# Optimization experiments

Measured on AMD Instinct MI355X. Metric: run time of the kernel, lower is better.

## Reference

```python
import jax, jax.numpy as jnp
from jax import lax
import numpy as np

# pywt db5 decomposition low-pass filter
_DB5 = np.array([0.003335725285001549, -0.012580751999015526, -0.006241490213011705,
                 0.07757149384006515, -0.03224486958502952, -0.24229488706619015,
                 0.13842814590110342, 0.7243085284385744, 0.6038292697974729,
                 0.160102397974125], dtype=np.float32)
_L = 10       # filter length (db5)
_LEVELS = 5   # decomp_level
_NT = 15      # SURE tuning grid size


def _filters():
    dec_lo = jnp.asarray(_DB5)
    sign = jnp.asarray(((-1.0) ** (np.arange(_L) + 1)).astype(np.float32))
    dec_hi = sign * dec_lo[::-1]          # QMF: g[k] = (-1)^(k+1) h[L-1-k]
    return dec_lo, dec_hi, dec_lo[::-1], dec_hi[::-1]


def _dwt1d(x, dlo, dhi):
    # x: (B, N) -> (B, 2, floor((N+L-1)/2)); pywt 'symmetric' convention
    p = _L - 1
    xe = jnp.pad(x, ((0, 0), (p, p)), mode='symmetric')[:, 1:]
    k = jnp.stack([dlo[::-1], dhi[::-1]])[:, None, :]  # (2,1,L), true convolution
    return lax.conv_general_dilated(xe[:, None, :], k, (2,), 'VALID',
                                    dimension_numbers=('NCH', 'OIH', 'NCH'))


def _idwt1d(a, d, rlo, rhi, n_out):
    # a,d: (B, M) -> (B, n_out); zero-upsample via lhs_dilation, full conv, crop L-2
    k = jnp.stack([rlo[::-1], rhi[::-1]])[None, :, :]  # (1,2,L)
    y = lax.conv_general_dilated(jnp.stack([a, d], axis=1), k, (1,),
                                 [(_L - 1, _L - 1)], lhs_dilation=(2,),
                                 dimension_numbers=('NCH', 'OIH', 'NCH'))
    return y[:, 0, _L - 2:_L - 2 + n_out]


def _dwt2_level(x, dlo, dhi):
    # x: (C, H, W) -> ll (C,Hd,Wd), highs (C,3,Hd,Wd)
    C, H, W = x.shape
    yw = _dwt1d(x.reshape(C * H, W), dlo, dhi).reshape(C, H, 2, -1)
    Wd = yw.shape[-1]
    yw = yw.transpose(0, 2, 3, 1)  # (C, wband, Wd, H)
    yh = _dwt1d(yw.reshape(C * 2 * Wd, H), dlo, dhi).reshape(C, 2, Wd, 2, -1)
    yh = yh.transpose(0, 1, 3, 4, 2)  # (C, wband, hband, Hd, Wd)
    ll = yh[:, 0, 0]
    highs = jnp.stack([yh[:, 0, 1], yh[:, 1, 0], yh[:, 1, 1]], axis=1)
    return ll, highs


def _idwt2_level(ll, highs, rlo, rhi, h_out, w_out):
    C, Hd, Wd = ll.shape
    lh, hl, hh = highs[:, 0], highs[:, 1], highs[:, 2]

    def inv_h(a, d):  # inverse along H axis
        at = a.transpose(0, 2, 1).reshape(C * Wd, Hd)
        dt = d.transpose(0, 2, 1).reshape(C * Wd, Hd)
        r = _idwt1d(at, dt, rlo, rhi, h_out)
        return r.reshape(C, Wd, h_out).transpose(0, 2, 1)

    lo_w = inv_h(ll, lh)
    hi_w = inv_h(hl, hh)
    r = _idwt1d(lo_w.reshape(C * h_out, Wd), hi_w.reshape(C * h_out, Wd),
                rlo, rhi, w_out)
    return r.reshape(C, h_out, w_out)


def _est_additive_noise(data):
    eps = 1e-6
    C = data.shape[0]
    ddp = data @ data.T
    ddpi = jnp.linalg.inv(ddp + eps * jnp.eye(C, dtype=data.dtype))

    def per_band(i):
        xx = ddpi - jnp.outer(ddpi[:, i], ddpi[i, :]) / ddpi[i, i]
        ddpa = ddp[:, i].at[i].set(0.0)
        beta = (xx @ ddpa).at[i].set(0.0)
        return data[i] - beta @ data

    return jax.vmap(per_band)(jnp.arange(C))


def _hyres(x, min_iter):
    dlo, dhi, rlo, rhi = _filters()
    H, W, C = x.shape
    N = H * W
    # 1) noise estimation -> per-band noise power omega1
    w = _est_additive_noise(x.reshape(N, C).T)               # (C, N)
    omega1 = (jnp.sqrt(jnp.var(w, axis=1, ddof=1)) + 1e-30) ** 2  # (C,)
    y_w = x * omega1 ** -0.5
    # 2) PCA: y_w2d = (U*S) @ Vh ; pc = scores as image cube
    u, s, vh = jnp.linalg.svd(y_w.reshape(N, C), full_matrices=False)
    pc = (u * s).reshape(H, W, C).transpose(2, 0, 1)         # (C, H, W)
    # 3) multi-level 2D DWT per band
    xmax, xmin = x.max(), x.min()
    ll = pc
    highs, sizes = [], []
    for _ in range(_LEVELS):
        sizes.append(ll.shape[1:])
        ll, hi = _dwt2_level(ll, dlo, dhi)
        highs.append(hi)
    ll = jnp.nan_to_num(ll, nan=0.0, posinf=xmax, neginf=xmin)
    highs = [jnp.nan_to_num(h, nan=0.0, posinf=xmax, neginf=xmin) for h in highs]
    # 4) flatten all coefficients -> (M, C)
    flat = [ll.reshape(C, -1)] + [h.reshape(C, -1) for h in highs]
    vperm = jnp.concatenate(flat, axis=1).T
    M = vperm.shape[0]
    norm2 = jnp.sum(vperm * vperm)
    K = norm2 - float(M * C)
    # 5) per-band SURE over a fixed threshold grid (vectorized over bands)
    x2 = vperm ** 2
    t_max = float(np.sqrt(np.log(M)))
    t_grid = jnp.linspace(0.0, t_max, _NT)

    def sure_at(t):
        t2 = t * t
        cnt = jnp.sum(x2 >= t2, axis=0).astype(vperm.dtype)
        sm = jnp.sum(jnp.minimum(x2, t2), axis=0)
        return sm + 2.0 * cnt - float(M)

    sure_all = jax.vmap(sure_at)(t_grid)                     # (NT, C)
    # 6) cumulative SURE recurrence S_r = sum_{j<r} S_j + a_r + K ; min over grid

    def step(cum, a_r):
        s_r = cum + a_r + K
        return cum + s_r, jnp.min(s_r)

    _, min_sure = lax.scan(step, jnp.zeros(_NT, vperm.dtype), sure_all.T)
    prev = jnp.concatenate([min_sure[:1], min_sure[:-1]])
    idx = jnp.arange(C)
    cond = (idx > min_iter) & jnp.logical_not(min_sure > 2.0 * prev)
    rank = jnp.where(jnp.any(cond), jnp.argmax(cond), C - 1)
    # 7) keep bands < rank (zeroing == slicing since iDWT/matmul are per-band linear)
    keep = (idx < rank).astype(vperm.dtype)
    ll_k = ll * keep[:, None, None]
    highs_k = [h * keep[:, None, None, None] for h in highs]
    y_est = ll_k
    for hi, (h_out, w_out) in zip(reversed(highs_k), reversed(sizes)):
        y_est = _idwt2_level(y_est, hi, rlo, rhi, h_out, w_out)
    y2d = y_est.transpose(1, 2, 0).reshape(N, C)
    y_restored = ((omega1 ** 0.5) * (y2d @ vh).reshape(H, W, C))
    return y_restored


def setup_inputs() -> dict:
    key = jax.random.key(0)
    x = jax.random.uniform(key, (256, 256, 191), dtype=jnp.float32)
    return {"x": x, "min_iter": 2}


def reference(x, min_iter):
    return _hyres(x, min_iter)
```

## Files before the change

kernel.cpp:

```cpp
#include <hip/hip_runtime.h>
#include <math.h>
#include <cstdint>

#define CH 191
#define NPIX 65536
#define MCOEF 74287
#define CSTRIDE 74288
#define SW32 4
#define NSKEW (96 * 194)

__device__ const float g_dlo[10] = {
  0.003335725285001549f, -0.012580751999015526f, -0.006241490213011705f,
  0.07757149384006515f, -0.03224486958502952f, -0.24229488706619015f,
  0.13842814590110342f, 0.7243085284385744f, 0.6038292697974729f,
  0.160102397974125f };
__device__ const float g_dhi[10] = {
  -0.160102397974125f, 0.6038292697974729f, -0.7243085284385744f,
  0.13842814590110342f, 0.24229488706619015f, -0.03224486958502952f,
  -0.07757149384006515f, -0.006241490213011705f, 0.012580751999015526f,
  0.003335725285001549f };

struct TArgs { double t2[15]; };

__device__ __forceinline__ int sk(int a, int b) {
  int s = a + b; if (s >= CH) s -= CH;
  int d = a - b; if (d < 0) d = -d;
  int df = (d > 95) ? (CH - d) : d;
  return df * 194 + s;
}

#define BAR_LGKM() asm volatile("s_waitcnt lgkmcnt(0)\n\ts_barrier" ::: "memory")

__global__ __launch_bounds__(256) void k_ddp(const float* __restrict__ x,
                                             double* __restrict__ ddp) {
  __shared__ float as[32][33];
  __shared__ float bs[32][33];
  int i0 = blockIdx.x * 32, j0 = blockIdx.y * 32;
  if (j0 < i0) return;
  int t = threadIdx.x;
  int n0 = blockIdx.z * 4096;
  int tx = t & 15, ty = t >> 4;
  double a00 = 0, a01 = 0, a10 = 0, a11 = 0;
  for (int nb = 0; nb < 4096; nb += 32) {
    for (int e = t; e < 1024; e += 256) {
      int kk = e >> 5, ii = e & 31;
      int n = n0 + nb + kk;
      as[kk][ii] = (i0 + ii < CH) ? x[(size_t)n * CH + i0 + ii] : 0.f;
      bs[kk][ii] = (j0 + ii < CH) ? x[(size_t)n * CH + j0 + ii] : 0.f;
    }
    __syncthreads();
    #pragma unroll 8
    for (int kk = 0; kk < 32; ++kk) {
      double x0 = as[kk][tx], x1 = as[kk][tx + 16];
      double y0 = bs[kk][ty], y1 = bs[kk][ty + 16];
      a00 += x0 * y0; a01 += x0 * y1; a10 += x1 * y0; a11 += x1 * y1;
    }
    __syncthreads();
  }
  int i = i0 + tx, j = j0 + ty;
  if (i < CH) {
    if (j < CH)      atomicAdd(&ddp[i * CH + j], a00);
    if (j + 16 < CH) atomicAdd(&ddp[i * CH + j + 16], a01);
  }
  if (i + 16 < CH) {
    if (j < CH)      atomicAdd(&ddp[(i + 16) * CH + j], a10);
    if (j + 16 < CH) atomicAdd(&ddp[(i + 16) * CH + j + 16], a11);
  }
}

__global__ void k_mirror(double* __restrict__ ddp) {
  int e = blockIdx.x * 256 + threadIdx.x;
  if (e >= CH * CH) return;
  int i = e / CH, j = e % CH;
  if (i > j) ddp[e] = ddp[j * CH + i];
}

__global__ __launch_bounds__(256) void k_rsum(const float* __restrict__ x,
                                              double* __restrict__ rsum) {
  int t = threadIdx.x;
  if (t >= CH) return;
  int row0 = blockIdx.x * 256;
  double a = 0;
  for (int r = 0; r < 256; ++r) a += (double)x[(size_t)(row0 + r) * CH + t];
  atomicAdd(&rsum[t], a);
}

__global__ __launch_bounds__(768) void k_gj(const double* __restrict__ ddp,
                                            float* __restrict__ out) {
  __shared__ float fc[192];
  int t = threadIdx.x;
  int i = t % 192;
  int cg = t / 192;
  int j0 = cg * 48;
  bool act = (i < CH);
  float a[48];
  #pragma unroll
  for (int m = 0; m < 48; ++m) {
    int j = j0 + m;
    a[m] = (act && j < CH) ? (float)(ddp[i * CH + j] + ((i == j) ? 1e-6 : 0.0)) : 0.f;
  }
  if (t < 192) fc[t] = 0.f;
  __syncthreads();
  for (int k = 0; k < CH; ++k) {
    int cgk = k / 48;
    int mk = k - cgk * 48;
    if (cg == cgk && act) {
      float v = 0.f;
      #pragma unroll
      for (int m = 0; m < 48; ++m) v = (m == mk) ? a[m] : v;
      fc[i] = v;
    }
    __syncthreads();
    float dinv = 1.0f / fc[k];
    float fci = fc[i];
    bool iskrow = (i == k);
    float s = fci * dinv;
    float colv = iskrow ? (-dinv) : s;
    #pragma unroll
    for (int mq = 0; mq < 12; ++mq) {
      float4 f4 = *(const float4*)&fc[j0 + mq * 4];
      #pragma unroll
      for (int c4 = 0; c4 < 4; ++c4) {
        int m = mq * 4 + c4;
        float fj = (c4 == 0) ? f4.x : (c4 == 1) ? f4.y : (c4 == 2) ? f4.z : f4.w;
        float gen = iskrow ? (fj * dinv) : (a[m] - s * fj);
        bool iskcol = (cg == cgk) && (m == mk);
        a[m] = iskcol ? colv : gen;
      }
    }
    __syncthreads();
  }
  if (act) {
    #pragma unroll
    for (int m = 0; m < 48; ++m) {
      int j = j0 + m;
      if (j < CH) out[i * CH + j] = -a[m];
    }
  }
}

__global__ void k_newton1(const double* __restrict__ ddp, const float* __restrict__ X,
                          double* __restrict__ T) {
  int j = blockIdx.x * 16 + threadIdx.x, i = blockIdx.y * 16 + threadIdx.y;
  if (i >= CH || j >= CH) return;
  double acc = 0;
  for (int k = 0; k < CH; ++k) {
    double a = ddp[i * CH + k] + (i == k ? 1e-6 : 0.0);
    acc += a * (double)X[k * CH + j];
  }
  T[i * CH + j] = (i == j ? 2.0 : 0.0) - acc;
}
__global__ void k_newton2(const float* __restrict__ X, const double* __restrict__ T,
                          double* __restrict__ P) {
  int j = blockIdx.x * 16 + threadIdx.x, i = blockIdx.y * 16 + threadIdx.y;
  if (i >= CH || j >= CH) return;
  double acc = 0;
  for (int k = 0; k < CH; ++k) acc += (double)X[i * CH + k] * T[k * CH + j];
  P[i * CH + j] = acc;
}

__global__ __launch_bounds__(256) void k_beta(const double* __restrict__ ddp,
                                              const double* __restrict__ P,
                                              const double* __restrict__ rsum,
                                              double* __restrict__ sqrtom,
                                              double* __restrict__ invs) {
  __shared__ double bet[CH];
  __shared__ double red[256];
  int i = blockIdx.x, t = threadIdx.x;
  double pii = P[i * CH + i];
  for (int j = t; j < CH; j += 256) {
    double pjip = P[j * CH + i] / pii;
    double acc = 0;
    for (int k = 0; k < CH; ++k) {
      double ddpa = (k == i) ? 0.0 : ddp[k * CH + i];
      acc += (P[j * CH + k] - pjip * P[i * CH + k]) * ddpa;
    }
    bet[j] = (j == i) ? 0.0 : acc;
  }
  __syncthreads();
  double s1 = 0, s2 = 0;
  for (int j = t; j < CH; j += 256) {
    double gj = ((j == i) ? 1.0 : 0.0) - bet[j];
    s1 += gj * rsum[j];
    double tj = 0;
    for (int k = 0; k < CH; ++k) {
      double gk = ((k == i) ? 1.0 : 0.0) - bet[k];
      tj += ddp[j * CH + k] * gk;
    }
    s2 += gj * tj;
  }
  red[t] = s1; __syncthreads();
  for (int o = 128; o; o >>= 1) { if (t < o) red[t] += red[t + o]; __syncthreads(); }
  double sumw = red[0]; __syncthreads();
  red[t] = s2; __syncthreads();
  for (int o = 128; o; o >>= 1) { if (t < o) red[t] += red[t + o]; __syncthreads(); }
  if (t == 0) {
    double sumsq = red[0];
    double var = (sumsq - sumw * sumw / 65536.0) / 65535.0;
    if (var < 0) var = 0;
    double so = sqrt(var) + 1e-30;
    sqrtom[i] = so;
    invs[i] = 1.0 / so;
  }
}

__global__ void k_packG(const double* __restrict__ ddp, const double* __restrict__ invs,
                        float* __restrict__ Gsk, float* __restrict__ dgf,
                        double* __restrict__ G64) {
  int e = blockIdx.x * 256 + threadIdx.x;
  if (e >= CH * CH) return;
  int i = e / CH, j = e % CH;
  double v = ddp[e] * invs[i] * invs[j];
  G64[e] = v;
  if (j >= i) Gsk[sk(i, j)] = (float)v;
  if (j == i) dgf[i] = (float)v;
}

__global__ __launch_bounds__(1024) void k_jac32(const float* __restrict__ Gsk,
                                                const float* __restrict__ dg0,
                                                float2* __restrict__ rlogA) {
  extern __shared__ float As[];
  __shared__ float2 csn[96];
  __shared__ float dg[CH];
  int t = threadIdx.x;

  int jS[5], kS[5]; int ntask = 0;
  for (int id = t; id < 4560; id += 1024) {
    int j = 0, off = 0;
    while (off + (95 - j) <= id) { off += 95 - j; ++j; }
    jS[ntask] = j; kS[ntask] = j + 1 + (id - off);
    ++ntask;
  }
  int a00[5], a01[5], a10[5], a11[5], limA[5], limB[5];
  #pragma unroll
  for (int ii = 0; ii < 5; ++ii) {
    if (ii < ntask) {
      int j = jS[ii], k = kS[ii];
      int A = j + k;
      int B = k - j;
      int dfB = (A > 95) ? (CH - A) : A;
      int bA = B * 194;
      int bB = dfB * 194;
      a00[ii] = (bA + A) * 4;
      a11[ii] = (bA + CH - A) * 4;
      a01[ii] = (bB + CH - B) * 4;
      a10[ii] = (bB + B) * 4;
      limA[ii] = (bA + CH) * 4;
      limB[ii] = (bB + CH) * 4;
    } else {
      a00[ii] = a01[ii] = a10[ii] = a11[ii] = 0;
      limA[ii] = limB[ii] = 1 << 30; jS[ii] = 0; kS[ii] = 1;
    }
  }

  for (int e = t; e < NSKEW; e += 1024) As[e] = Gsk[e];
  if (t < CH) dg[t] = dg0[t];
  __syncthreads();

  const char* Asb = (const char*)As;
  for (int sweep = 0; sweep < SW32; ++sweep) {
    for (int r = 0; r < CH; ++r) {
      float m0[5], m1[5], m2[5], m3[5];
      #pragma unroll
      for (int ii = 0; ii < 5; ++ii) {
        if (ii < ntask) {
          m0[ii] = *(const float*)(Asb + a00[ii]);
          m1[ii] = *(const float*)(Asb + a01[ii]);
          if (jS[ii] != 0) {
            m2[ii] = *(const float*)(Asb + a10[ii]);
            m3[ii] = *(const float*)(Asb + a11[ii]);
          }
        }
      }
      if (t >= 1 && t < 96) {
        int p = r + t; if (p >= CH) p -= CH;
        int q = r - t; if (q < 0) q += CH;
        int ipq = sk(p, q);
        float app = dg[p], aqq = dg[q], apq = As[ipq];
        float c = 1.0f, s = 0.0f, piv = apq, dp = app, dq = aqq;
        if (fabsf(apq) > 3e-7f * (fabsf(app) + fabsf(aqq)) + 1e-30f) {
          float tau = (aqq - app) / (2.0f * apq);
          float tt = copysignf(1.0f, tau) / (fabsf(tau) + sqrtf(1.0f + tau * tau));
          c = 1.0f / sqrtf(1.0f + tt * tt); s = tt * c;
          dp = app - tt * apq; dq = aqq + tt * apq; piv = 0.0f;
        }
        dg[p] = dp; dg[q] = dq;
        As[ipq] = piv;
        csn[t] = make_float2(c, s);
        rlogA[((size_t)(sweep * CH + r)) * 95 + (t - 1)] = make_float2(c, s);
      }
      BAR_LGKM();
      #pragma unroll
      for (int ii = 0; ii < 5; ++ii) {
        if (ii < ntask) {
          float2 ck2 = csn[kS[ii]];
          if (jS[ii] == 0) {
            float vp = m0[ii], vq = m1[ii];
            *(float*)((char*)As + a00[ii]) = ck2.x * vp - ck2.y * vq;
            *(float*)((char*)As + a01[ii]) = ck2.y * vp + ck2.x * vq;
          } else {
            float2 cj2 = csn[jS[ii]];
            float n00 = ck2.x * m0[ii] - ck2.y * m1[ii];
            float n01 = ck2.y * m0[ii] + ck2.x * m1[ii];
            float n10 = ck2.x * m2[ii] - ck2.y * m3[ii];
            float n11 = ck2.y * m2[ii] + ck2.x * m3[ii];
            *(float*)((char*)As + a00[ii]) = cj2.x * n00 - cj2.y * n10;
            *(float*)((char*)As + a10[ii]) = cj2.y * n00 + cj2.x * n10;
            *(float*)((char*)As + a01[ii]) = cj2.x * n01 - cj2.y * n11;
            *(float*)((char*)As + a11[ii]) = cj2.y * n01 + cj2.x * n11;
          }
          a00[ii] += 8; if (a00[ii] >= limA[ii]) a00[ii] -= 764;
          a11[ii] += 8; if (a11[ii] >= limA[ii]) a11[ii] -= 764;
          a01[ii] += 8; if (a01[ii] >= limB[ii]) a01[ii] -= 764;
          a10[ii] += 8; if (a10[ii] >= limB[ii]) a10[ii] -= 764;
        }
      }
      BAR_LGKM();
    }
  }
}

__global__ __launch_bounds__(128) void k_replayA(const float2* __restrict__ rlogA,
                                                 double* __restrict__ Q) {
  __shared__ double vr[CH];
  int row = blockIdx.x, t = threadIdx.x;
  const int NR = SW32 * CH;
  for (int j = t; j < CH; j += 128) vr[j] = (j == row) ? 1.0 : 0.0;
  bool act = (t < 95);
  float2 nb[4];
  #pragma unroll
  for (int u = 0; u < 4; ++u)
    nb[u] = (act && u < NR) ? rlogA[(size_t)u * 95 + t] : make_float2(1.f, 0.f);
  BAR_LGKM();
  int r = 0;
  for (int g = 0; g < NR; g += 4) {
    #pragma unroll
    for (int u = 0; u < 4; ++u) {
      float2 cur = nb[u];
      int gn = g + u + 4;
      nb[u] = (act && gn < NR) ? rlogA[(size_t)gn * 95 + t] : make_float2(1.f, 0.f);
      if (act && cur.y != 0.f) {
        int k = t + 1;
        int p = r + k; if (p >= CH) p -= CH;
        int q = r - k; if (q < 0) q += CH;
        double s = (double)cur.y;
        double c = sqrt(fmax(0.0, 1.0 - s * s));
        double vp = vr[p], vq = vr[q];
        vr[p] = c * vp - s * vq;
        vr[q] = s * vp + c * vq;
      }
      if (++r == CH) r = 0;
      BAR_LGKM();
    }
  }
  for (int j = t; j < CH; j += 128) Q[(size_t)row * CH + j] = vr[j];
}

__global__ void k_gq(const double* __restrict__ G64, const double* __restrict__ Q,
                     double* __restrict__ T) {
  int j = blockIdx.x * 16 + threadIdx.x, i = blockIdx.y * 16 + threadIdx.y;
  if (i >= CH || j >= CH) return;
  double acc = 0;
  for (int k = 0; k < CH; ++k) acc += G64[i * CH + k] * Q[(size_t)k * CH + j];
  T[i * CH + j] = acc;
}
__global__ void k_qtq(const double* __restrict__ Q, const double* __restrict__ T,
                      double* __restrict__ A2sk, double* __restrict__ dg64) {
  int j = blockIdx.x * 16 + threadIdx.x, i = blockIdx.y * 16 + threadIdx.y;
  if (i >= CH || j >= CH || j < i) return;
  double acc = 0;
  for (int k = 0; k < CH; ++k) acc += Q[(size_t)k * CH + i] * T[k * CH + j];
  if (j == i) dg64[i] = acc;
  else A2sk[sk(i, j)] = acc;
}

__global__ __launch_bounds__(1024) void k_jac64(const double* __restrict__ A2sk,
                                                const double* __restrict__ dg0,
                                                double* __restrict__ eig,
                                                double2* __restrict__ rlogB) {
  extern __shared__ double As64[];
  __shared__ double2 csn[96];
  __shared__ double dg[CH];
  int t = threadIdx.x;

  int jS[5], kS[5]; int ntask = 0;
  for (int id = t; id < 4560; id += 1024) {
    int j = 0, off = 0;
    while (off + (95 - j) <= id) { off += 95 - j; ++j; }
    jS[ntask] = j; kS[ntask] = j + 1 + (id - off);
    ++ntask;
  }
  int a00[5], a01[5], a10[5], a11[5], limA[5], limB[5];
  #pragma unroll
  for (int ii = 0; ii < 5; ++ii) {
    if (ii < ntask) {
      int j = jS[ii], k = kS[ii];
      int A = j + k;
      int B = k - j;
      int dfB = (A > 95) ? (CH - A) : A;
      int bA = B * 194;
      int bB = dfB * 194;
      a00[ii] = (bA + A) * 8;
      a11[ii] = (bA + CH - A) * 8;
      a01[ii] = (bB + CH - B) * 8;
      a10[ii] = (bB + B) * 8;
      limA[ii] = (bA + CH) * 8;
      limB[ii] = (bB + CH) * 8;
    } else {
      a00[ii] = a01[ii] = a10[ii] = a11[ii] = 0;
      limA[ii] = limB[ii] = 1 << 30; jS[ii] = 0; kS[ii] = 1;
    }
  }

  for (int e = t; e < NSKEW; e += 1024) As64[e] = A2sk[e];
  if (t < CH) dg[t] = dg0[t];
  __syncthreads();

  const char* Asb = (const char*)As64;
  for (int r = 0; r < CH; ++r) {
    double m0[5], m1[5], m2[5], m3[5];
    #pragma unroll
    for (int ii = 0; ii < 5; ++ii) {
      if (ii < ntask) {
        m0[ii] = *(const double*)(Asb + a00[ii]);
        m1[ii] = *(const double*)(Asb + a01[ii]);
        if (jS[ii] != 0) {
          m2[ii] = *(const double*)(Asb + a10[ii]);
          m3[ii] = *(const double*)(Asb + a11[ii]);
        }
      }
    }
    if (t >= 1 && t < 96) {
      int p = r + t; if (p >= CH) p -= CH;
      int q = r - t; if (q < 0) q += CH;
      int ipq = sk(p, q);
      double app = dg[p], aqq = dg[q], apq = As64[ipq];
      double c = 1.0, s = 0.0, piv = apq, dp = app, dq = aqq;
      if (fabs(apq) > 4e-16 * (fabs(app) + fabs(aqq)) + 1e-300) {
        double tau = (aqq - app) / (2.0 * apq);
        double tt = copysign(1.0, tau) / (fabs(tau) + sqrt(1.0 + tau * tau));
        c = 1.0 / sqrt(1.0 + tt * tt); s = tt * c;
        dp = app - tt * apq; dq = aqq + tt * apq; piv = 0.0;
      }
      dg[p] = dp; dg[q] = dq;
      As64[ipq] = piv;
      csn[t] = make_double2(c, s);
      rlogB[(size_t)r * 95 + (t - 1)] = make_double2(c, s);
    }
    BAR_LGKM();
    #pragma unroll
    for (int ii = 0; ii < 5; ++ii) {
      if (ii < ntask) {
        double2 ck2 = csn[kS[ii]];
        if (jS[ii] == 0) {
          double vp = m0[ii], vq = m1[ii];
          *(double*)((char*)As64 + a00[ii]) = ck2.x * vp - ck2.y * vq;
          *(double*)((char*)As64 + a01[ii]) = ck2.y * vp + ck2.x * vq;
        } else {
          double2 cj2 = csn[jS[ii]];
          double n00 = ck2.x * m0[ii] - ck2.y * m1[ii];
          double n01 = ck2.y * m0[ii] + ck2.x * m1[ii];
          double n10 = ck2.x * m2[ii] - ck2.y * m3[ii];
          double n11 = ck2.y * m2[ii] + ck2.x * m3[ii];
          *(double*)((char*)As64 + a00[ii]) = cj2.x * n00 - cj2.y * n10;
          *(double*)((char*)As64 + a10[ii]) = cj2.y * n00 + cj2.x * n10;
          *(double*)((char*)As64 + a01[ii]) = cj2.x * n01 - cj2.y * n11;
          *(double*)((char*)As64 + a11[ii]) = cj2.y * n01 + cj2.x * n11;
        }
        a00[ii] += 16; if (a00[ii] >= limA[ii]) a00[ii] -= 1528;
        a11[ii] += 16; if (a11[ii] >= limA[ii]) a11[ii] -= 1528;
        a01[ii] += 16; if (a01[ii] >= limB[ii]) a01[ii] -= 1528;
        a10[ii] += 16; if (a10[ii] >= limB[ii]) a10[ii] -= 1528;
      }
    }
    BAR_LGKM();
  }
  for (int i = t; i < CH; i += 1024) eig[i] = dg[i];
}

__global__ __launch_bounds__(128) void k_replayB(const double2* __restrict__ rlogB,
                                                 const double* __restrict__ Q,
                                                 double* __restrict__ V) {
  __shared__ double vr[CH];
  int row = blockIdx.x, t = threadIdx.x;
  const int NR = CH;
  for (int j = t; j < CH; j += 128) vr[j] = Q[(size_t)row * CH + j];
  double2 nxt = (t < 95) ? rlogB[t] : make_double2(1.0, 0.0);
  BAR_LGKM();
  for (int g = 0; g < NR; ++g) {
    double2 cur = nxt;
    if (t < 95 && g + 1 < NR) nxt = rlogB[(size_t)(g + 1) * 95 + t];
    if (t < 95 && cur.y != 0.0) {
      int k = t + 1;
      int p = g + k; if (p >= CH) p -= CH;
      int q = g - k; if (q < 0) q += CH;
      double vp = vr[p], vq = vr[q];
      vr[p] = cur.x * vp - cur.y * vq;
      vr[q] = cur.y * vp + cur.x * vq;
    }
    BAR_LGKM();
  }
  for (int j = t; j < CH; j += 128) V[(size_t)row * CH + j] = vr[j];
}

__global__ __launch_bounds__(256) void k_sortprep(const double* __restrict__ eig,
                                                  const double* __restrict__ V,
                                                  const double* __restrict__ invs,
                                                  int* __restrict__ perm,
                                                  float* __restrict__ Vw) {
  __shared__ double ev[CH];
  __shared__ int pm[CH];
  int t = threadIdx.x;
  if (t < CH) ev[t] = eig[t];
  __syncthreads();
  if (t < CH) {
    double my = ev[t];
    int rk = 0;
    for (int j = 0; j < CH; ++j) {
      double o = ev[j];
      rk += (o > my || (o == my && j < t)) ? 1 : 0;
    }
    pm[rk] = t;
  }
  __syncthreads();
  if (t < CH) perm[t] = pm[t];
  for (int e = t; e < 192 * 192; e += 256) {
    int k = e / 192, i = e - k * 192;
    float v = 0.f;
    if (k < CH && i < CH) v = (float)(invs[k] * V[(size_t)k * CH + pm[i]]);
    Vw[e] = v;
  }
}

__global__ __launch_bounds__(256) void k_pc(const float* __restrict__ x,
                                            const float* __restrict__ Vw,
                                            float* __restrict__ pcT) {
  __shared__ float xs[16][65];
  __shared__ float vs[16][33];
  int n0 = blockIdx.x * 64, i0 = blockIdx.y * 32;
  int t = threadIdx.x;
  int tn = t & 15, ti = t >> 4;
  float acc[4][2] = {};
  for (int k0 = 0; k0 < 192; k0 += 16) {
    {
      int col = t & 15, row = t >> 4;
      #pragma unroll
      for (int rr = 0; rr < 4; ++rr) {
        int nn = row + rr * 16;
        int k = k0 + col;
        xs[col][nn] = (k < CH) ? x[(size_t)(n0 + nn) * CH + k] : 0.f;
      }
    }
    {
      int ii = t & 31, kk = t >> 5;
      vs[kk][ii] = Vw[(k0 + kk) * 192 + i0 + ii];
      vs[kk + 8][ii] = Vw[(k0 + kk + 8) * 192 + i0 + ii];
    }
    __syncthreads();
    #pragma unroll
    for (int kk = 0; kk < 16; ++kk) {
      float b0 = vs[kk][ti], b1 = vs[kk][ti + 16];
      #pragma unroll
      for (int rr = 0; rr < 4; ++rr) {
        float a = xs[kk][tn + rr * 16];
        acc[rr][0] += a * b0;
        acc[rr][1] += a * b1;
      }
    }
    __syncthreads();
  }
  #pragma unroll
  for (int rr = 0; rr < 4; ++rr)
    #pragma unroll
    for (int bb = 0; bb < 2; ++bb) {
      int i = i0 + ti + bb * 16, n = n0 + tn + rr * 16;
      if (i < CH) pcT[(size_t)i * NPIX + n] = acc[rr][bb];
    }
}

__global__ __launch_bounds__(256) void k_row(const float* __restrict__ in,
                                             float* __restrict__ rb,
                                             int h, int w, int wd, int chS) {
  __shared__ float rowv[256];
  int bid = blockIdx.x;
  int c = bid / h, y = bid % h;
  const float* src = in + (size_t)c * chS + (size_t)y * w;
  int t = threadIdx.x;
  if (t < w) rowv[t] = src[t];
  __syncthreads();
  float* dst = rb + (size_t)(c * h + y) * (2 * wd);
  for (int o = t; o < 2 * wd; o += 256) {
    int b = (o >= wd) ? 1 : 0;
    int xp = b ? o - wd : o;
    float acc = 0.f;
    #pragma unroll
    for (int s = 0; s < 10; ++s) {
      int m = 2 * xp + 1 - s;
      if (m < 0) m = -1 - m;
      else if (m >= w) m = 2 * w - 1 - m;
      acc += (b ? g_dhi[s] : g_dlo[s]) * rowv[m];
    }
    dst[o] = acc;
  }
}

__global__ __launch_bounds__(256) void k_col(const float* __restrict__ rb,
                                             float* __restrict__ llout,
                                             float* __restrict__ coeff,
                                             int h, int wd, int hd, int chSout,
                                             int offHi, int offLL, int lastlvl) {
  int c = blockIdx.z, yp = blockIdx.y;
  int xq = blockIdx.x * 256 + threadIdx.x;
  if (xq >= 2 * wd) return;
  const float* base = rb + (size_t)c * h * 2 * wd + xq;
  float lo = 0.f, hi = 0.f;
  #pragma unroll
  for (int s = 0; s < 10; ++s) {
    int m = 2 * yp + 1 - s;
    if (m < 0) m = -1 - m;
    else if (m >= h) m = 2 * h - 1 - m;
    float v = base[(size_t)m * 2 * wd];
    lo += g_dlo[s] * v;
    hi += g_dhi[s] * v;
  }
  float* cc = coeff + (size_t)c * CSTRIDE;
  if (xq < wd) {
    llout[(size_t)c * chSout + (size_t)yp * wd + xq] = lo;
    if (lastlvl) cc[offLL + yp * wd + xq] = lo;
    cc[offHi + 0 * hd * wd + yp * wd + xq] = hi;
  } else {
    int xp = xq - wd;
    cc[offHi + 1 * hd * wd + yp * wd + xp] = lo;
    cc[offHi + 2 * hd * wd + yp * wd + xp] = hi;
  }
}

__global__ __launch_bounds__(256) void k_stats(const float* __restrict__ coeff,
                                               double* __restrict__ stats, TArgs ta) {
  int c = blockIdx.y;
  const float* cc = coeff + (size_t)c * CSTRIDE;
  double sm[15], cnt[15], nrm = 0;
  #pragma unroll
  for (int q = 0; q < 15; ++q) { sm[q] = 0; cnt[q] = 0; }
  for (int idx = blockIdx.x * 256 + threadIdx.x; idx < MCOEF; idx += 24 * 256) {
    double v = (double)cc[idx];
    double v2 = v * v;
    nrm += v2;
    #pragma unroll
    for (int q = 0; q < 15; ++q) {
      sm[q] += fmin(v2, ta.t2[q]);
      cnt[q] += (v2 >= ta.t2[q]) ? 1.0 : 0.0;
    }
  }
  __shared__ double wred[4][31];
  int lane = threadIdx.x & 63, wv = threadIdx.x >> 6;
  for (int q = 0; q < 31; ++q) {
    double val = (q < 15) ? sm[q] : ((q < 30) ? cnt[q - 15] : nrm);
    #pragma unroll
    for (int o = 32; o > 0; o >>= 1) val += __shfl_down(val, o);
    if (lane == 0) wred[wv][q] = val;
  }
  __syncthreads();
  if (threadIdx.x < 31) {
    double sum = wred[0][threadIdx.x] + wred[1][threadIdx.x] +
                 wred[2][threadIdx.x] + wred[3][threadIdx.x];
    atomicAdd(&stats[c * 31 + threadIdx.x], sum);
  }
}

__global__ __launch_bounds__(256) void k_sure(const double* __restrict__ stats,
                                              const double* __restrict__ sqrtom,
                                              const double* __restrict__ V,
                                              const int* __restrict__ perm,
                                              const int* __restrict__ min_iter_p,
                                              float* __restrict__ Wm,
                                              int* __restrict__ meta) {
  __shared__ double st[CH * 31];
  __shared__ double minsure[CH];
  __shared__ int rankS;
  int t = threadIdx.x;
  for (int e = t; e < CH * 31; e += 256) st[e] = stats[e];
  __syncthreads();
  if (t == 0) {
    double norm2 = 0;
    for (int c = 0; c < CH; ++c) norm2 += st[c * 31 + 30];
    double K = norm2 - (double)MCOEF * (double)CH;
    double cum[15];
    for (int q = 0; q < 15; ++q) cum[q] = 0;
    for (int r = 0; r < CH; ++r) {
      double mn = 1e300;
      for (int q = 0; q < 15; ++q) {
        double sure = st[r * 31 + q] + 2.0 * st[r * 31 + 15 + q] - (double)MCOEF;
        double s = cum[q] + sure + K;
        cum[q] += s;
        if (s < mn) mn = s;
      }
      minsure[r] = mn;
    }
    int mi = *min_iter_p;
    int rank = CH - 1;
    for (int r = 0; r < CH; ++r) {
      double prev = (r == 0) ? minsure[0] : minsure[r - 1];
      bool cond = (r > mi) && !(minsure[r] > 2.0 * prev);
      if (cond) { rank = r; break; }
    }
    rankS = rank;
    meta[1] = rank;
  }
  __syncthreads();
  int rank = rankS;
  for (int e = t; e < 192 * 192; e += 256) {
    int k = e / 192, c = e - k * 192;
    float v = 0.f;
    if (k < rank && c < CH) v = (float)(sqrtom[c] * V[(size_t)c * CH + perm[k]]);
    Wm[e] = v;
  }
}

__global__ __launch_bounds__(256) void k_out(const float* __restrict__ pcT,
                                             const float* __restrict__ Wm,
                                             float* __restrict__ out) {
  __shared__ float psx[16][65];
  __shared__ float wsx[16][33];
  int n0 = blockIdx.x * 64, c0 = blockIdx.y * 32;
  int t = threadIdx.x;
  int tc = t & 15, tn = t >> 4;
  float acc[4][2] = {};
  for (int k0 = 0; k0 < 192; k0 += 16) {
    {
      int nn = t & 63, kk0 = t >> 6;
      #pragma unroll
      for (int rr = 0; rr < 4; ++rr) {
        int kk = kk0 + rr * 4;
        int k = k0 + kk;
        psx[kk][nn] = (k < CH) ? pcT[(size_t)k * NPIX + n0 + nn] : 0.f;
      }
    }
    {
      int cc = t & 31, kk = t >> 5;
      wsx[kk][cc] = Wm[(k0 + kk) * 192 + c0 + cc];
      wsx[kk + 8][cc] = Wm[(k0 + kk + 8) * 192 + c0 + cc];
    }
    __syncthreads();
    #pragma unroll
    for (int kk = 0; kk < 16; ++kk) {
      float b0 = wsx[kk][tc], b1 = wsx[kk][tc + 16];
      #pragma unroll
      for (int rr = 0; rr < 4; ++rr) {
        float a = psx[kk][tn + rr * 16];
        acc[rr][0] += a * b0;
        acc[rr][1] += a * b1;
      }
    }
    __syncthreads();
  }
  #pragma unroll
  for (int rr = 0; rr < 4; ++rr)
    #pragma unroll
    for (int bb = 0; bb < 2; ++bb) {
      int n = n0 + tn + rr * 16, c = c0 + tc + bb * 16;
      if (c < CH) out[(size_t)n * CH + c] = acc[rr][bb];
    }
}

extern "C" void kernel_launch(void* const* d_in, const int* in_sizes, int n_in,
                              void* d_out, int out_size, void* d_ws, size_t ws_size,
                              hipStream_t stream) {
  const float* x = (const float*)d_in[0];
  const int* p_min_iter = (const int*)d_in[1];
  float* out = (float*)d_out;
  char* ws = (char*)d_ws;

  size_t cur = 0;
  auto A = [&](size_t b) { size_t o = cur; cur += (b + 511) & ~(size_t)511; return o; };
  double* ddp     = (double*)(ws + A((size_t)CH * CH * 8));
  double* ddpi64  = (double*)(ws + A((size_t)CH * CH * 8));
  double* Tm      = (double*)(ws + A((size_t)CH * CH * 8));
  double* V       = (double*)(ws + A((size_t)CH * CH * 8));
  double* G64     = (double*)(ws + A((size_t)CH * CH * 8));
  double* T64     = (double*)(ws + A((size_t)CH * CH * 8));
  double* Q       = (double*)(ws + A((size_t)CH * CH * 8));
  double* A2sk    = (double*)(ws + A((size_t)NSKEW * 8));
  double* dg64    = (double*)(ws + A((size_t)CH * 8));
  double* eig     = (double*)(ws + A((size_t)CH * 8));
  double* rsum    = (double*)(ws + A((size_t)CH * 8));
  double* sqrtom  = (double*)(ws + A((size_t)CH * 8));
  double* invs    = (double*)(ws + A((size_t)CH * 8));
  double* stats   = (double*)(ws + A((size_t)CH * 31 * 8));
  int* perm       = (int*)(ws + A((size_t)CH * 4));
  int* meta       = (int*)(ws + A(64));
  float* ddpi32   = (float*)(ws + A((size_t)CH * CH * 4));
  float* Gsk      = (float*)(ws + A((size_t)NSKEW * 4));
  float* dgf      = (float*)(ws + A((size_t)CH * 4));
  float* Vw       = (float*)(ws + A((size_t)192 * 192 * 4));
  float* Wm       = (float*)(ws + A((size_t)192 * 192 * 4));
  float2* rlogA   = (float2*)(ws + A((size_t)SW32 * CH * 95 * 8));
  double2* rlogB  = (double2*)(ws + A((size_t)CH * 95 * 16));
  float* pcT      = (float*)(ws + A((size_t)CH * NPIX * 4));
  float* rowbuf   = (float*)(ws + A((size_t)CH * 256 * 264 * 4));
  float* llA      = (float*)(ws + A((size_t)CH * 17424 * 4));
  float* llB      = (float*)(ws + A((size_t)CH * 4900 * 4));
  float* coeff    = (float*)(ws + A((size_t)CH * CSTRIDE * 4));
  (void)ws_size; (void)in_sizes; (void)n_in; (void)out_size;

  hipMemsetAsync(ddp, 0, (size_t)CH * CH * 8, stream);
  hipMemsetAsync(rsum, 0, (size_t)CH * 8, stream);
  hipMemsetAsync(stats, 0, (size_t)CH * 31 * 8, stream);

  const int J32_SMEM = NSKEW * 4;
  const int J64_SMEM = NSKEW * 8;

  k_ddp<<<dim3(6, 6, 16), 256, 0, stream>>>(x, ddp);
  k_mirror<<<143, 256, 0, stream>>>(ddp);
  k_rsum<<<256, 256, 0, stream>>>(x, rsum);
  k_gj<<<1, 768, 0, stream>>>(ddp, ddpi32);
  k_newton1<<<dim3(12, 12), dim3(16, 16), 0, stream>>>(ddp, ddpi32, Tm);
  k_newton2<<<dim3(12, 12), dim3(16, 16), 0, stream>>>(ddpi32, Tm, ddpi64);
  k_beta<<<CH, 256, 0, stream>>>(ddp, ddpi64, rsum, sqrtom, invs);
  k_packG<<<143, 256, 0, stream>>>(ddp, invs, Gsk, dgf, G64);
  (void)hipFuncSetAttribute((const void*)k_jac32,
        hipFuncAttributeMaxDynamicSharedMemorySize, J32_SMEM);
  k_jac32<<<1, 1024, J32_SMEM, stream>>>(Gsk, dgf, rlogA);
  k_replayA<<<CH, 128, 0, stream>>>(rlogA, Q);
  k_gq<<<dim3(12, 12), dim3(16, 16), 0, stream>>>(G64, Q, T64);
  k_qtq<<<dim3(12, 12), dim3(16, 16), 0, stream>>>(Q, T64, A2sk, dg64);
  (void)hipFuncSetAttribute((const void*)k_jac64,
        hipFuncAttributeMaxDynamicSharedMemorySize, J64_SMEM);
  k_jac64<<<1, 1024, J64_SMEM, stream>>>(A2sk, dg64, eig, rlogB);
  k_replayB<<<CH, 128, 0, stream>>>(rlogB, Q, V);
  k_sortprep<<<1, 256, 0, stream>>>(eig, V, invs, perm, Vw);
  k_pc<<<dim3(1024, 6), 256, 0, stream>>>(x, Vw, pcT);

  int hs[6] = {256, 132, 70, 39, 24, 16};
  int offHi[5];
  { int a0 = 0; for (int l = 0; l < 5; ++l) { offHi[l] = a0; a0 += 3 * hs[l + 1] * hs[l + 1]; } }
  const int offLL = 74031;
  float* lls[6] = {pcT, llA, llB, llA, llB, llA};
  for (int l = 0; l < 5; ++l) {
    int h = hs[l], w = hs[l], wd = hs[l + 1], hd = hs[l + 1];
    k_row<<<CH * h, 256, 0, stream>>>(lls[l], rowbuf, h, w, wd, h * w);
    k_col<<<dim3((2 * wd + 255) / 256, hd, CH), 256, 0, stream>>>(
        rowbuf, lls[l + 1], coeff, h, wd, hd, hd * wd, offHi[l], offLL,
        (l == 4) ? 1 : 0);
  }

  TArgs ta;
  {
    double tmax = sqrt(log((double)MCOEF));
    for (int j = 0; j < 15; ++j) { double tv = tmax * j / 14.0; ta.t2[j] = tv * tv; }
  }
  k_stats<<<dim3(24, CH), 256, 0, stream>>>(coeff, stats, ta);
  k_sure<<<1, 256, 0, stream>>>(stats, sqrtom, V, perm, p_min_iter, Wm, meta);
  k_out<<<dim3(1024, 6), 256, 0, stream>>>(pcT, Wm, out);
}
```

Before: 3.680 ms.

## Fuse DWT levels 2-5 into one per-channel shared-memory kernel

Wavelet levels 2 through 5 previously took two kernel launches each (row pass and column pass), with every intermediate going through global memory. They now run in a single kernel with one block per channel, holding the LL image and the row-filtered buffer in LDS and writing only the coefficients to global memory. This removes eight launches and their global round-trips. In exchange, only 191 blocks run, each using about 140KB of LDS, so occupancy and parallelism on these smaller levels are low.

```diff
diff --git a/kernel.cpp b/kernel.cpp
--- a/kernel.cpp
+++ b/kernel.cpp
@@ -632,6 +632,63 @@
     int xp = xq - wd;
     cc[offHi + 1 * hd * wd + yp * wd + xp] = lo;
     cc[offHi + 2 * hd * wd + yp * wd + xp] = hi;
+  }
+}
+
+#define DWT_SMEM ((17424 + 18480) * 4)
+__global__ __launch_bounds__(256) void k_dwt_tail(const float* __restrict__ llin,
+                                                  float* __restrict__ coeff) {
+  extern __shared__ float smem[];
+  float* A = smem;
+  float* B = smem + 17424;
+  const int hsz[5]   = {132, 70, 39, 24, 16};
+  const int offHiC[4] = {52272, 66972, 71535, 73263};
+  int c = blockIdx.x, t = threadIdx.x;
+  float* cc = coeff + (size_t)c * CSTRIDE;
+  for (int e = t; e < 132 * 132; e += 256) A[e] = llin[(size_t)c * 17424 + e];
+  BAR_LGKM();
+  #pragma unroll
+  for (int l = 0; l < 4; ++l) {
+    const int h = hsz[l], w = hsz[l], wd = hsz[l + 1], hd = hsz[l + 1];
+    const int w2 = 2 * wd;
+    for (int e = t; e < h * w2; e += 256) {
+      int y = e / w2, o = e - y * w2;
+      int b = (o >= wd) ? 1 : 0;
+      int xp = b ? o - wd : o;
+      float acc = 0.f;
+      #pragma unroll
+      for (int s = 0; s < 10; ++s) {
+        int m = 2 * xp + 1 - s;
+        if (m < 0) m = -1 - m;
+        else if (m >= w) m = 2 * w - 1 - m;
+        acc += (b ? g_dhi[s] : g_dlo[s]) * A[y * w + m];
+      }
+      B[y * w2 + o] = acc;
+    }
+    BAR_LGKM();
+    for (int e = t; e < hd * w2; e += 256) {
+      int yp = e / w2, xq = e - yp * w2;
+      float lo = 0.f, hi = 0.f;
+      #pragma unroll
+      for (int s = 0; s < 10; ++s) {
+        int m = 2 * yp + 1 - s;
+        if (m < 0) m = -1 - m;
+        else if (m >= h) m = 2 * h - 1 - m;
+        float v = B[m * w2 + xq];
+        lo += g_dlo[s] * v;
+        hi += g_dhi[s] * v;
+      }
+      if (xq < wd) {
+        A[yp * wd + xq] = lo;
+        if (l == 3) cc[74031 + yp * wd + xq] = lo;
+        cc[offHiC[l] + 0 * hd * wd + yp * wd + xq] = hi;
+      } else {
+        int xp = xq - wd;
+        cc[offHiC[l] + 1 * hd * wd + yp * wd + xp] = lo;
+        cc[offHiC[l] + 2 * hd * wd + yp * wd + xp] = hi;
+      }
+    }
+    BAR_LGKM();
   }
 }
 
@@ -799,7 +856,6 @@
   float* pcT      = (float*)(ws + A((size_t)CH * NPIX * 4));
   float* rowbuf   = (float*)(ws + A((size_t)CH * 256 * 264 * 4));
   float* llA      = (float*)(ws + A((size_t)CH * 17424 * 4));
-  float* llB      = (float*)(ws + A((size_t)CH * 4900 * 4));
   float* coeff    = (float*)(ws + A((size_t)CH * CSTRIDE * 4));
   (void)ws_size; (void)in_sizes; (void)n_in; (void)out_size;
 
@@ -831,18 +887,12 @@
   k_sortprep<<<1, 256, 0, stream>>>(eig, V, invs, perm, Vw);
   k_pc<<<dim3(1024, 6), 256, 0, stream>>>(x, Vw, pcT);
 
-  int hs[6] = {256, 132, 70, 39, 24, 16};
-  int offHi[5];
-  { int a0 = 0; for (int l = 0; l < 5; ++l) { offHi[l] = a0; a0 += 3 * hs[l + 1] * hs[l + 1]; } }
-  const int offLL = 74031;
-  float* lls[6] = {pcT, llA, llB, llA, llB, llA};
-  for (int l = 0; l < 5; ++l) {
-    int h = hs[l], w = hs[l], wd = hs[l + 1], hd = hs[l + 1];
-    k_row<<<CH * h, 256, 0, stream>>>(lls[l], rowbuf, h, w, wd, h * w);
-    k_col<<<dim3((2 * wd + 255) / 256, hd, CH), 256, 0, stream>>>(
-        rowbuf, lls[l + 1], coeff, h, wd, hd, hd * wd, offHi[l], offLL,
-        (l == 4) ? 1 : 0);
-  }
+  k_row<<<CH * 256, 256, 0, stream>>>(pcT, rowbuf, 256, 256, 132, NPIX);
+  k_col<<<dim3(2, 132, CH), 256, 0, stream>>>(
+      rowbuf, llA, coeff, 256, 132, 132, 132 * 132, 0, 74031, 0);
+  (void)hipFuncSetAttribute((const void*)k_dwt_tail,
+        hipFuncAttributeMaxDynamicSharedMemorySize, DWT_SMEM);
+  k_dwt_tail<<<CH, 256, DWT_SMEM, stream>>>(llA, coeff);
 
   TArgs ta;
   {
```

Result: no change. 3.670 ms, median of 2 (-0.3%).
